# Performance work log

Measured on AMD Instinct MI355X. Metric: run time of the kernel, lower is better.

Reference implementation:

```python
import jax, jax.numpy as jnp
import numpy as np


def _idct_tables():
    steps = jnp.arange(8, dtype=jnp.float32) / 16.0
    f = 2.0 * jnp.arange(8, dtype=jnp.float32) + 1.0
    h = jnp.cos(jnp.outer(steps, f * jnp.pi))            # [u, x]
    # basis[x, y, u, v] = h[u, x] * h[v, y]
    basis = h.T[:, None, :, None] * h.T[None, :, None, :]
    c = jnp.ones(8, dtype=jnp.float32).at[0].set(jnp.sqrt(jnp.float32(0.5)))
    scale = 0.25 * jnp.outer(c, c)                        # [u, v]
    return basis, scale


def setup_inputs() -> dict:
    key = jax.random.key(0)
    dct = jax.random.normal(key, (16, 64, 256, 256), dtype=jnp.float32)
    mean = jnp.zeros(64, dtype=jnp.float32)
    std = jnp.ones(64, dtype=jnp.float32)
    return {"dct": dct, "mean": mean, "std": std}


def reference(dct, mean, std):
    B, C, H, W = dct.shape  # C == 64
    basis, scale = _idct_tables()
    # destandardize per DCT coefficient
    d = dct * std[None, :, None, None] + mean[None, :, None, None]
    d = d.reshape(B, 8, 8, H, W)  # (B, u, v, H, W)
    # 2D IDCT: sum over u, v of scale[u,v] * basis[x,y,u,v] * d[b,u,v,h,w]
    # (mathematically equal to the original's broadcasted outer-product sum)
    res = jnp.einsum('uv,xyuv,buvhw->bxyhw', scale, basis, d)
    # interleave block pixels into full image: (B, H, x, W, y) -> (B, 1, 8H, 8W)
    res = jnp.transpose(res, (0, 3, 1, 4, 2)).reshape(B, 1, 8 * H, 8 * W)
    return (res + 128.0) / 255.0
```

## Files before the change

kernel.cpp:

```cpp
#include <hip/hip_runtime.h>

__device__ __constant__ float G[64] = {
    0.3535533906f,  0.3535533906f,  0.3535533906f,  0.3535533906f,
    0.3535533906f,  0.3535533906f,  0.3535533906f,  0.3535533906f,

    0.4903926402f,  0.4157348062f,  0.2777851165f,  0.0975451610f,
   -0.0975451610f, -0.2777851165f, -0.4157348062f, -0.4903926402f,

    0.4619397663f,  0.1913417162f, -0.1913417162f, -0.4619397663f,
   -0.4619397663f, -0.1913417162f,  0.1913417162f,  0.4619397663f,

    0.4157348062f, -0.0975451610f, -0.4903926402f, -0.2777851165f,
    0.2777851165f,  0.4903926402f,  0.0975451610f, -0.4157348062f,

    0.3535533906f, -0.3535533906f, -0.3535533906f,  0.3535533906f,
    0.3535533906f, -0.3535533906f, -0.3535533906f,  0.3535533906f,

    0.2777851165f, -0.4903926402f,  0.0975451610f,  0.4157348062f,
   -0.4157348062f, -0.0975451610f,  0.4903926402f, -0.2777851165f,

    0.1913417162f, -0.4619397663f,  0.4619397663f, -0.1913417162f,
   -0.1913417162f,  0.4619397663f, -0.4619397663f,  0.1913417162f,

    0.0975451610f, -0.2777851165f,  0.4157348062f, -0.4903926402f,
    0.4903926402f, -0.4157348062f,  0.2777851165f, -0.0975451610f,
};

__global__ __launch_bounds__(256) void idct_kernel(
    const float* __restrict__ dct,
    const float* __restrict__ mean_,
    const float* __restrict__ std_,
    float* __restrict__ out)
{
    const int gid = blockIdx.x * 256 + threadIdx.x;
    const int w = gid & 255;
    const int h = (gid >> 8) & 255;
    const int b = gid >> 16;

    const float* p = dct + (size_t)b * 64 * 65536 + (size_t)h * 256 + (size_t)w;

    float t[8][8];
#pragma unroll
    for (int x = 0; x < 8; ++x)
#pragma unroll
        for (int v = 0; v < 8; ++v) t[x][v] = 0.0f;

#pragma unroll
    for (int u = 0; u < 8; ++u) {
#pragma unroll
        for (int v = 0; v < 8; ++v) {
            const int c = u * 8 + v;
            const float raw = p[(size_t)c * 65536];
            const float dv = fmaf(raw, std_[c], mean_[c]);
#pragma unroll
            for (int x = 0; x < 8; ++x)
                t[x][v] = fmaf(G[u * 8 + x], dv, t[x][v]);
        }
    }

    const float inv255 = 1.0f / 255.0f;
    const float off128 = 128.0f / 255.0f;

    const size_t obase = (size_t)b * (2048u * 2048u) + (size_t)(h * 8) * 2048 + (size_t)(w * 8);

#pragma unroll
    for (int x = 0; x < 8; ++x) {
        float pix[8];
#pragma unroll
        for (int y = 0; y < 8; ++y) {
            float s = 0.0f;
#pragma unroll
            for (int v = 0; v < 8; ++v)
                s = fmaf(G[v * 8 + y], t[x][v], s);
            pix[y] = fmaf(s, inv255, off128);
        }
        float4* o = (float4*)(out + obase + (size_t)x * 2048);
        o[0] = make_float4(pix[0], pix[1], pix[2], pix[3]);
        o[1] = make_float4(pix[4], pix[5], pix[6], pix[7]);
    }
}

extern "C" void kernel_launch(void* const* d_in, const int* in_sizes, int n_in,
                              void* d_out, int out_size, void* d_ws, size_t ws_size,
                              hipStream_t stream) {
    const float* dct  = (const float*)d_in[0];
    const float* mean = (const float*)d_in[1];
    const float* std_ = (const float*)d_in[2];
    float* out = (float*)d_out;

    const int total_threads = 16 * 256 * 256;
    const int block = 256;
    const int grid = total_threads / block;
    idct_kernel<<<grid, block, 0, stream>>>(dct, mean, std_, out);
}
```

Before: 435.8 us.

## Stage DCT tile in LDS via direct global-to-LDS loads, split rows across two threads

Each block now stages a 64-channel by 128-pixel tile of coefficients into shared memory using asynchronous global_load_lds 16-byte copies. Two threads then share each 8x8 block, each producing four output rows, using the even/odd symmetry of the IDCT basis (sign flip for odd u, mirrored row index). The constant table is made constexpr so its values fold into immediates. This halves the per-thread register state and arithmetic and vectorises the loads, at the cost of a barrier and 32 KB of LDS per block, which limits occupancy.

```diff
diff --git a/kernel.cpp b/kernel.cpp
--- a/kernel.cpp
+++ b/kernel.cpp
@@ -1,6 +1,6 @@
 #include <hip/hip_runtime.h>
 
-__device__ __constant__ float G[64] = {
+__device__ constexpr float G[64] = {
     0.3535533906f,  0.3535533906f,  0.3535533906f,  0.3535533906f,
     0.3535533906f,  0.3535533906f,  0.3535533906f,  0.3535533906f,
 
@@ -26,55 +26,83 @@
     0.4903926402f, -0.4157348062f,  0.2777851165f, -0.0975451610f,
 };
 
+#define WB 128
+
+typedef __attribute__((address_space(1))) const void gvoid_t;
+typedef __attribute__((address_space(3))) void lvoid_t;
+
 __global__ __launch_bounds__(256) void idct_kernel(
     const float* __restrict__ dct,
     const float* __restrict__ mean_,
     const float* __restrict__ std_,
     float* __restrict__ out)
 {
-    const int gid = blockIdx.x * 256 + threadIdx.x;
-    const int w = gid & 255;
-    const int h = (gid >> 8) & 255;
-    const int b = gid >> 16;
+    __shared__ __align__(16) float sh[64 * WB];
 
-    const float* p = dct + (size_t)b * 64 * 65536 + (size_t)h * 256 + (size_t)w;
+    const int t   = threadIdx.x;
+    const int blk = blockIdx.x;
+    const int wh  = blk & 1;
+    const int h   = (blk >> 1) & 255;
+    const int b   = blk >> 9;
+    const int w0  = wh * WB;
 
-    float t[8][8];
+    const float* gbase = dct + ((size_t)b << 22) + ((size_t)h << 8) + w0;
 #pragma unroll
-    for (int x = 0; x < 8; ++x)
+    for (int k = 0; k < 8; ++k) {
+        const int idx = k * 256 + t;
+        const int c   = idx >> 5;
+        const int wq  = idx & 31;
+        const float* gp = gbase + ((size_t)c << 16) + (wq << 2);
+        __builtin_amdgcn_global_load_lds((gvoid_t*)gp,
+                                         (lvoid_t*)(sh + (size_t)idx * 4),
+                                         16, 0, 0);
+    }
+    __syncthreads();
+
+    const int j  = t & (WB - 1);
+    const int xh = t >> 7;
+    const unsigned sgn = (unsigned)xh << 31;
+
+    float acc[4][8];
 #pragma unroll
-        for (int v = 0; v < 8; ++v) t[x][v] = 0.0f;
+    for (int xi = 0; xi < 4; ++xi)
+#pragma unroll
+        for (int v = 0; v < 8; ++v) acc[xi][v] = 0.0f;
 
 #pragma unroll
     for (int u = 0; u < 8; ++u) {
 #pragma unroll
         for (int v = 0; v < 8; ++v) {
             const int c = u * 8 + v;
-            const float raw = p[(size_t)c * 65536];
-            const float dv = fmaf(raw, std_[c], mean_[c]);
+            const float raw = sh[c * WB + j];
+            const float dv  = fmaf(raw, std_[c], mean_[c]);
+            const float dvs = __uint_as_float(__float_as_uint(dv) ^ sgn);
+            const float dsel = (u & 1) ? dvs : dv;
 #pragma unroll
-            for (int x = 0; x < 8; ++x)
-                t[x][v] = fmaf(G[u * 8 + x], dv, t[x][v]);
+            for (int xi = 0; xi < 4; ++xi)
+                acc[xi][v] = fmaf(G[u * 8 + xi], dsel, acc[xi][v]);
         }
     }
 
     const float inv255 = 1.0f / 255.0f;
     const float off128 = 128.0f / 255.0f;
 
-    const size_t obase = (size_t)b * (2048u * 2048u) + (size_t)(h * 8) * 2048 + (size_t)(w * 8);
+    const size_t orow0 = ((size_t)b << 22) + ((size_t)(h * 8) << 11)
+                       + (size_t)((w0 + j) * 8);
 
 #pragma unroll
-    for (int x = 0; x < 8; ++x) {
+    for (int xi = 0; xi < 4; ++xi) {
+        const int x = xi ^ (xh * 7);
         float pix[8];
 #pragma unroll
         for (int y = 0; y < 8; ++y) {
             float s = 0.0f;
 #pragma unroll
             for (int v = 0; v < 8; ++v)
-                s = fmaf(G[v * 8 + y], t[x][v], s);
+                s = fmaf(G[v * 8 + y], acc[xi][v], s);
             pix[y] = fmaf(s, inv255, off128);
         }
-        float4* o = (float4*)(out + obase + (size_t)x * 2048);
+        float4* o = (float4*)(out + orow0 + ((size_t)x << 11));
         o[0] = make_float4(pix[0], pix[1], pix[2], pix[3]);
         o[1] = make_float4(pix[4], pix[5], pix[6], pix[7]);
     }
@@ -88,8 +116,6 @@
     const float* std_ = (const float*)d_in[2];
     float* out = (float*)d_out;
 
-    const int total_threads = 16 * 256 * 256;
-    const int block = 256;
-    const int grid = total_threads / block;
-    idct_kernel<<<grid, block, 0, stream>>>(dct, mean, std_, out);
+    const int grid = 16 * 256 * 2;
+    idct_kernel<<<grid, 256, 0, stream>>>(dct, mean, std_, out);
 }
```

Result: no change. 432.5 us (-0.7%).
